# Kernel tuning notes

Hardware: AMD Instinct MI355X
Metric: run time of the kernel (lower is better)

## Reference

```python
import jax, jax.numpy as jnp
import numpy as np

EMB = 1024
NUM_HEADS = 16


def setup_inputs() -> dict:
    key = jax.random.key(0)
    k_x, k_k, k_q, k_v, k_u, k_b = jax.random.split(key, 6)
    b, s, e = 4, 2048, EMB
    lim = 1.0 / np.sqrt(e)
    return {
        "x": jax.random.normal(k_x, (b, s, e), dtype=jnp.float32),
        "Wk": jax.random.uniform(k_k, (e, e), jnp.float32, -lim, lim),
        "Wq": jax.random.uniform(k_q, (e, e), jnp.float32, -lim, lim),
        "Wv": jax.random.uniform(k_v, (e, e), jnp.float32, -lim, lim),
        "Wu": jax.random.uniform(k_u, (e, e), jnp.float32, -lim, lim),
        "bu": jax.random.uniform(k_b, (e,), jnp.float32, -lim, lim),
    }


def reference(x, Wk, Wq, Wv, Wu, bu):
    b, s, e = x.shape
    h = NUM_HEADS
    d = e // h
    # scale q and k each by emb**(-1/4), as in the original (note: emb, not head_size)
    scale = e ** -0.25
    # project and split heads: (b, h, s, d)
    q = (x @ Wq.T).reshape(b, s, h, d).transpose(0, 2, 1, 3) * scale
    k = (x @ Wk.T).reshape(b, s, h, d).transpose(0, 2, 1, 3) * scale
    v = (x @ Wv.T).reshape(b, s, h, d).transpose(0, 2, 1, 3)
    # attention scores (b, h, s, s)
    dot = jnp.einsum("bhqd,bhkd->bhqk", q, k)
    # causal mask: strictly-upper triangle (offset=1) set to -inf
    causal = jnp.triu(jnp.ones((s, s), dtype=bool), k=1)
    dot = jnp.where(causal[None, None, :, :], -jnp.inf, dot)
    attn = jax.nn.softmax(dot, axis=-1)
    out = jnp.einsum("bhqk,bhkd->bhqd", attn, v)
    out = out.transpose(0, 2, 1, 3).reshape(b, s, e)
    return out @ Wu.T + bu
```

## Files before the change

kernel.cpp:

```cpp
#include <hip/hip_runtime.h>
#include <stdint.h>
#include <math.h>


typedef __attribute__((ext_vector_type(8))) short bf16x8;
typedef __attribute__((ext_vector_type(4))) float f32x4;
typedef __attribute__((ext_vector_type(16))) float f32x16;
typedef __attribute__((ext_vector_type(4))) int i32x4;
typedef __attribute__((ext_vector_type(4))) short s16x4;

#define GLOAD_LDS16(gp, lp)                                                     \
  __builtin_amdgcn_global_load_lds(                                             \
      (__attribute__((address_space(1))) void*)(gp),                            \
      (__attribute__((address_space(3))) void*)(lp), 16, 0, 0)

__device__ __forceinline__ short f2bf(float f) {
  union { float f; uint32_t u; } v; v.f = f;
  uint32_t r = v.u + 0x7FFFu + ((v.u >> 16) & 1u);
  return (short)(r >> 16);
}
__device__ __forceinline__ float bf2f(short s) {
  union { uint32_t u; float f; } v; v.u = ((uint32_t)(uint16_t)s) << 16;
  return v.f;
}
__device__ __forceinline__ short f2bfn(float f) {
  union { __bf16 h; short s; } u; u.h = (__bf16)f; return u.s;
}
__device__ __forceinline__ uint32_t pk2n(float a, float b) {
  union { __bf16 h[2]; uint32_t u; } v;
  v.h[0] = (__bf16)a; v.h[1] = (__bf16)b;
  return v.u;
}

__device__ __forceinline__ void swap32(uint32_t a, uint32_t b, int hi,
                                       uint32_t& out0, uint32_t& out1) {
#if __has_builtin(__builtin_amdgcn_permlane32_swap)
  typedef __attribute__((ext_vector_type(2))) int i32x2;
  i32x2 r = __builtin_amdgcn_permlane32_swap((int)a, (int)b, false, false);
  out0 = (uint32_t)r.x; out1 = (uint32_t)r.y;
#else
  uint32_t ta = (uint32_t)__shfl_xor((int)a, 32);
  uint32_t tb = (uint32_t)__shfl_xor((int)b, 32);
  out0 = hi ? tb : a;
  out1 = hi ? b : ta;
#endif
}

__global__ __launch_bounds__(256) void cast_kernel(const float* __restrict__ src,
                                                   short* __restrict__ dst, int n) {
  int i = (blockIdx.x * 256 + threadIdx.x) * 8;
  if (i >= n) return;
  const float4* s = (const float4*)(src + i);
  float4 f0 = s[0], f1 = s[1];
  bf16x8 o;
  o[0] = f2bf(f0.x); o[1] = f2bf(f0.y); o[2] = f2bf(f0.z); o[3] = f2bf(f0.w);
  o[4] = f2bf(f1.x); o[5] = f2bf(f1.y); o[6] = f2bf(f1.z); o[7] = f2bf(f1.w);
  *(bf16x8*)(dst + i) = o;
}

__global__ __launch_bounds__(256) void cast4_kernel(const float* __restrict__ w0,
                                                    const float* __restrict__ w1,
                                                    const float* __restrict__ w2,
                                                    const float* __restrict__ w3,
                                                    short* o0, short* o1, short* o2, short* o3) {
  const float* src = (blockIdx.y == 0) ? w0 : (blockIdx.y == 1) ? w1 : (blockIdx.y == 2) ? w2 : w3;
  short* dst = (blockIdx.y == 0) ? o0 : (blockIdx.y == 1) ? o1 : (blockIdx.y == 2) ? o2 : o3;
  int i = (blockIdx.x * 256 + threadIdx.x) * 8;
  const float4* s = (const float4*)(src + i);
  float4 f0 = s[0], f1 = s[1];
  bf16x8 o;
  o[0] = f2bf(f0.x); o[1] = f2bf(f0.y); o[2] = f2bf(f0.z); o[3] = f2bf(f0.w);
  o[4] = f2bf(f1.x); o[5] = f2bf(f1.y); o[6] = f2bf(f1.z); o[7] = f2bf(f1.w);
  *(bf16x8*)(dst + i) = o;
}

template <bool F32OUT>
__device__ __forceinline__ void gemm_bt_core(const short* __restrict__ A,
                                             const short* __restrict__ Bm,
                                             short* __restrict__ Cb,
                                             float* __restrict__ Cf,
                                             const float* __restrict__ bias) {
  __shared__ short a_lds[128 * 64];
  __shared__ short b_lds[128 * 64];
  const int tid = threadIdx.x;
  const int w = tid >> 6, l = tid & 63;
  const int l15 = l & 15, lhi = l >> 4;
  const int wr = w >> 1, wc = w & 1;
  const int row0 = blockIdx.x * 128;
  const int col0 = blockIdx.y * 128;

  f32x4 acc[4][4];
#pragma unroll
  for (int m = 0; m < 4; ++m)
#pragma unroll
    for (int n = 0; n < 4; ++n)
      acc[m][n] = (f32x4){0.f, 0.f, 0.f, 0.f};

  const int o0 = tid * 16;
  const int sr = o0 >> 7;
  const int sc = o0 & 127;

  for (int kt = 0; kt < 16; ++kt) {
    const char* Ab = (const char*)A + (size_t)(row0 + sr) * 2048 + kt * 128 + sc;
    const char* Bb = (const char*)Bm + (size_t)(col0 + sr) * 2048 + kt * 128 + sc;
#pragma unroll
    for (int i = 0; i < 4; ++i) {
      GLOAD_LDS16(Ab + (size_t)i * 32 * 2048, (char*)a_lds + i * 4096 + o0);
      GLOAD_LDS16(Bb + (size_t)i * 32 * 2048, (char*)b_lds + i * 4096 + o0);
    }
    __syncthreads();
#pragma unroll
    for (int kk = 0; kk < 2; ++kk) {
      bf16x8 af[4], bg[4];
#pragma unroll
      for (int m = 0; m < 4; ++m) {
        int r = wr * 64 + m * 16 + l15;
        af[m] = *(const bf16x8*)((const char*)a_lds + r * 128 + kk * 64 + lhi * 16);
      }
#pragma unroll
      for (int n = 0; n < 4; ++n) {
        int r = wc * 64 + n * 16 + l15;
        bg[n] = *(const bf16x8*)((const char*)b_lds + r * 128 + kk * 64 + lhi * 16);
      }
#pragma unroll
      for (int m = 0; m < 4; ++m)
#pragma unroll
        for (int n = 0; n < 4; ++n)
          acc[m][n] = __builtin_amdgcn_mfma_f32_16x16x32_bf16(af[m], bg[n], acc[m][n], 0, 0, 0);
    }
    __syncthreads();
  }

#pragma unroll
  for (int m = 0; m < 4; ++m) {
#pragma unroll
    for (int n = 0; n < 4; ++n) {
      int colg = col0 + wc * 64 + n * 16 + l15;
#pragma unroll
      for (int r = 0; r < 4; ++r) {
        int rowg = row0 + wr * 64 + m * 16 + lhi * 4 + r;
        float v = acc[m][n][r];
        if constexpr (F32OUT) {
          Cf[(size_t)rowg * 1024 + colg] = v + bias[colg];
        } else {
          Cb[(size_t)rowg * 1024 + colg] = f2bfn(v);
        }
      }
    }
  }
}

__global__ __launch_bounds__(256) void gemm_qkv_kernel(const short* __restrict__ xb,
                                                       const short* __restrict__ wq,
                                                       const short* __restrict__ wk,
                                                       const short* __restrict__ wv,
                                                       short* qo, short* ko, short* vo) {
  const short* Bm = (blockIdx.z == 0) ? wq : (blockIdx.z == 1) ? wk : wv;
  short* C = (blockIdx.z == 0) ? qo : (blockIdx.z == 1) ? ko : vo;
  gemm_bt_core<false>(xb, Bm, C, nullptr, nullptr);
}

__global__ __launch_bounds__(256) void gemm_out_kernel(const short* __restrict__ ob,
                                                       const short* __restrict__ wu,
                                                       const float* __restrict__ bias,
                                                       float* __restrict__ out) {
  gemm_bt_core<true>(ob, wu, nullptr, out, bias);
}

__global__ __launch_bounds__(256) void frag_qk_kernel(const short* __restrict__ qb,
                                                      const short* __restrict__ kb,
                                                      short* __restrict__ qf,
                                                      short* __restrict__ kf) {
  int t = blockIdx.x, bh = blockIdx.y;
  int b = bh >> 4, h = bh & 15;
  __shared__ short q_t[32][72], k_t[32][72];
  int tid = threadIdx.x;
  int row = tid >> 3, seg = tid & 7;
  size_t src = ((size_t)(b * 2048 + t * 32 + row)) * 1024 + h * 64 + seg * 8;
  *(bf16x8*)&q_t[row][seg * 8] = *(const bf16x8*)(qb + src);
  *(bf16x8*)&k_t[row][seg * 8] = *(const bf16x8*)(kb + src);
  __syncthreads();
  int s = tid >> 6, l = tid & 63, l31 = l & 31, hi = l >> 5;
  bf16x8 cq = *(const bf16x8*)&q_t[l31][hi * 8 + s * 16];
  bf16x8 ck = *(const bf16x8*)&k_t[l31][hi * 8 + s * 16];
  size_t dst = ((size_t)bh * 64 + t) * 2048 + s * 512 + l * 8;
  *(bf16x8*)(qf + dst) = cq;
  *(bf16x8*)(kf + dst) = ck;
}

__global__ __launch_bounds__(256) void frag_v_kernel(const short* __restrict__ vb,
                                                     short* __restrict__ vf) {
  int t = blockIdx.x, bh = blockIdx.y;
  int b = bh >> 4, h = bh & 15;
  __shared__ short v_t[32][72];
  int tid = threadIdx.x;
  int row = tid >> 3, seg = tid & 7;
  *(bf16x8*)&v_t[row][seg * 8] =
      *(const bf16x8*)(vb + ((size_t)(b * 2048 + t * 32 + row)) * 1024 + h * 64 + seg * 8);
  __syncthreads();
  int u = tid >> 6, l = tid & 63, l31 = l & 31, hi = l >> 5;
  int dblk = u >> 1, koff = u & 1;
  bf16x8 c;
#pragma unroll
  for (int j = 0; j < 8; ++j) c[j] = v_t[koff * 16 + hi * 8 + j][dblk * 32 + l31];
  *(bf16x8*)(vf + ((size_t)bh * 64 + t) * 2048 + u * 512 + l * 8) = c;
}

__global__ __launch_bounds__(512) void attn_kernel(const short* __restrict__ qf,
                                                   const short* __restrict__ kf,
                                                   const short* __restrict__ vf,
                                                   short* __restrict__ ob) {
  const float QSCALE = 0.03125f * 1.44269504f;
  int bh = blockIdx.x;
  int b = bh >> 4, h = bh & 15;
  int tid = threadIdx.x;
  int wid = tid >> 6, l = tid & 63;
  int l31 = l & 31, hi = l >> 5;
  int pair = blockIdx.y * 4 + (wid >> 1);
  int team = wid & 1;
  int slot = wid >> 1;

  __shared__ float mrg[4][64][34];

  const short* qfb = qf + (size_t)bh * 131072;
  const short* kfb = kf + (size_t)bh * 131072;
  const short* vfb = vf + (size_t)bh * 131072;

  for (int part = 0; part < 2; ++part) {
    int sidx = part ? (63 - pair) : pair;
    int qrow0 = sidx * 32;
    int qg = qrow0 + l31;
    int n = sidx + 1;
    int t0 = team ? (n >> 1) : 0;
    int t1 = team ? n : (n >> 1);

    bf16x8 aq[4];
    {
      const short* qp = qfb + sidx * 2048 + l * 8;
#pragma unroll
      for (int s = 0; s < 4; ++s) {
        bf16x8 t = *(const bf16x8*)(qp + s * 512);
#pragma unroll
        for (int jj = 0; jj < 8; ++jj) t[jj] = f2bfn(bf2f(t[jj]) * QSCALE);
        aq[s] = t;
      }
    }

    f32x16 o_lo = {}, o_hi = {};
    float lsum = 0.f;

    for (int t = t0; t < t1; ++t) {
      const short* kp = kfb + (size_t)t * 2048 + l * 8;
      const short* vp = vfb + (size_t)t * 2048 + l * 8;
      f32x16 st;
#pragma unroll
      for (int r = 0; r < 16; ++r) st[r] = -8.0f;
#pragma unroll
      for (int s = 0; s < 4; ++s) {
        bf16x8 ak = *(const bf16x8*)(kp + s * 512);
        st = __builtin_amdgcn_mfma_f32_32x32x16_bf16(ak, aq[s], st, 0, 0, 0);
      }

      if (t == sidx) {
#pragma unroll
        for (int r = 0; r < 16; ++r) {
          int kk = qrow0 + (r & 3) + 8 * (r >> 2) + 4 * hi;
          if (kk > qg) st[r] = -INFINITY;
        }
      }

#pragma unroll
      for (int r = 0; r < 16; ++r) st[r] = exp2f(st[r]);

      float sm[8];
#pragma unroll
      for (int r = 0; r < 8; ++r) sm[r] = st[r] + st[r + 8];
#pragma unroll
      for (int r = 0; r < 4; ++r) sm[r] += sm[r + 4];
      lsum += (sm[0] + sm[1]) + (sm[2] + sm[3]);

      uint32_t a0, a2, b1, b3, c0, c2, d1, d3;
      swap32(pk2n(st[0], st[1]),   pk2n(st[4], st[5]),   hi, a0, a2);
      swap32(pk2n(st[2], st[3]),   pk2n(st[6], st[7]),   hi, b1, b3);
      swap32(pk2n(st[8], st[9]),   pk2n(st[12], st[13]), hi, c0, c2);
      swap32(pk2n(st[10], st[11]), pk2n(st[14], st[15]), hi, d1, d3);
      i32x4 u0 = {(int)a0, (int)b1, (int)a2, (int)b3};
      i32x4 u1 = {(int)c0, (int)d1, (int)c2, (int)d3};
      bf16x8 pa0 = __builtin_bit_cast(bf16x8, u0);
      bf16x8 pa1 = __builtin_bit_cast(bf16x8, u1);

      bf16x8 av;
      av = *(const bf16x8*)(vp);
      o_lo = __builtin_amdgcn_mfma_f32_32x32x16_bf16(av, pa0, o_lo, 0, 0, 0);
      av = *(const bf16x8*)(vp + 512);
      o_lo = __builtin_amdgcn_mfma_f32_32x32x16_bf16(av, pa1, o_lo, 0, 0, 0);
      av = *(const bf16x8*)(vp + 1024);
      o_hi = __builtin_amdgcn_mfma_f32_32x32x16_bf16(av, pa0, o_hi, 0, 0, 0);
      av = *(const bf16x8*)(vp + 1536);
      o_hi = __builtin_amdgcn_mfma_f32_32x32x16_bf16(av, pa1, o_hi, 0, 0, 0);
    }

    lsum += __shfl_xor(lsum, 32);

    if (team == 1) {
      float* pp = &mrg[slot][l][0];
#pragma unroll
      for (int r = 0; r < 16; ++r) { pp[r] = o_lo[r]; pp[16 + r] = o_hi[r]; }
      pp[32] = lsum;
    }
    __syncthreads();
    if (team == 0) {
      const float* pp = &mrg[slot][l][0];
      float inv = 1.0f / (lsum + pp[32]);
      short* obase = ob + (size_t)(b * 2048 + qg) * 1024 + h * 64;
#pragma unroll
      for (int g = 0; g < 4; ++g) {
        int d0 = 8 * g + 4 * hi;
        s16x4 v0, v1;
#pragma unroll
        for (int jj = 0; jj < 4; ++jj) {
          v0[jj] = f2bfn((o_lo[4 * g + jj] + pp[4 * g + jj]) * inv);
          v1[jj] = f2bfn((o_hi[4 * g + jj] + pp[16 + 4 * g + jj]) * inv);
        }
        *(s16x4*)(obase + d0) = v0;
        *(s16x4*)(obase + 32 + d0) = v1;
      }
    }
    __syncthreads();
  }
}

extern "C" void kernel_launch(void* const* d_in, const int* in_sizes, int n_in,
                              void* d_out, int out_size, void* d_ws, size_t ws_size,
                              hipStream_t stream) {
  const float* x  = (const float*)d_in[0];
  const float* Wk = (const float*)d_in[1];
  const float* Wq = (const float*)d_in[2];
  const float* Wv = (const float*)d_in[3];
  const float* Wu = (const float*)d_in[4];
  const float* bu = (const float*)d_in[5];
  float* out = (float*)d_out;

  char* ws = (char*)d_ws;
  const size_t MB = 1u << 20;
  short* xb  = (short*)(ws + 0 * MB);
  short* qf  = (short*)(ws + 0 * MB);
  short* qb  = (short*)(ws + 16 * MB);
  short* vfb = (short*)(ws + 16 * MB);
  short* kb  = (short*)(ws + 32 * MB);
  short* vb  = (short*)(ws + 48 * MB);
  short* kfb = (short*)(ws + 64 * MB);
  short* ob  = (short*)(ws + 80 * MB);
  short* wqb = (short*)(ws + 96 * MB);
  short* wkb = (short*)(ws + 98 * MB);
  short* wvb = (short*)(ws + 100 * MB);
  short* wub = (short*)(ws + 102 * MB);

  cast_kernel<<<4096, 256, 0, stream>>>(x, xb, 8388608);
  cast4_kernel<<<dim3(512, 4), 256, 0, stream>>>(Wq, Wk, Wv, Wu, wqb, wkb, wvb, wub);

  gemm_qkv_kernel<<<dim3(64, 8, 3), 256, 0, stream>>>(xb, wqb, wkb, wvb, qb, kb, vb);
  frag_qk_kernel<<<dim3(64, 64), 256, 0, stream>>>(qb, kb, qf, kfb);
  frag_v_kernel<<<dim3(64, 64), 256, 0, stream>>>(vb, vfb);
  attn_kernel<<<dim3(64, 8), 512, 0, stream>>>(qf, kfb, vfb, ob);
  gemm_out_kernel<<<dim3(64, 8), 256, 0, stream>>>(ob, wub, bu, out);
}
```

Before: 198.3 us.

## Fuse fragment relayout and Q scaling into QKV GEMM epilogue, prefetch K/V in attention

The QKV GEMM epilogue now writes Q, K and V straight into the MFMA fragment layouts the attention kernel expects, and applies the softmax scale to Q there. This removes the two separate relayout kernels and their extra global round trip, plus the per-element Q rescaling inside attention. The attention loop also software-prefetches the next K tile and loads the V tile before the score MFMAs, so load latency overlaps compute. The cost is scattered 2-byte stores in the GEMM epilogue instead of coalesced row stores, and Q is now rounded to bf16 once after scaling rather than twice.

```diff
diff --git a/kernel.cpp b/kernel.cpp
--- a/kernel.cpp
+++ b/kernel.cpp
@@ -74,12 +74,13 @@
   *(bf16x8*)(dst + i) = o;
 }
 
-template <bool F32OUT>
+template <int MODE>
 __device__ __forceinline__ void gemm_bt_core(const short* __restrict__ A,
                                              const short* __restrict__ Bm,
                                              short* __restrict__ Cb,
                                              float* __restrict__ Cf,
                                              const float* __restrict__ bias) {
+  const float QSCALE = 0.03125f * 1.44269504f;
   __shared__ short a_lds[128 * 64];
   __shared__ short b_lds[128 * 64];
   const int tid = threadIdx.x;
@@ -140,10 +141,24 @@
       for (int r = 0; r < 4; ++r) {
         int rowg = row0 + wr * 64 + m * 16 + lhi * 4 + r;
         float v = acc[m][n][r];
-        if constexpr (F32OUT) {
+        if constexpr (MODE == 3) {
           Cf[(size_t)rowg * 1024 + colg] = v + bias[colg];
         } else {
-          Cb[(size_t)rowg * 1024 + colg] = f2bfn(v);
+          int b = rowg >> 11, srow = rowg & 2047;
+          int t = srow >> 5;
+          int h = colg >> 6, d = colg & 63;
+          size_t base = ((size_t)((b << 4) + h) * 64 + t) << 11;
+          if constexpr (MODE == 2) {
+            int rr = srow & 31;
+            size_t idx = base + (size_t)(((d >> 5) << 1) + (rr >> 4)) * 512 +
+                         (size_t)((((rr >> 3) & 1) << 5) + (d & 31)) * 8 + (rr & 7);
+            Cb[idx] = f2bfn(v);
+          } else {
+            int l31r = srow & 31;
+            size_t idx = base + (size_t)(d >> 4) * 512 +
+                         (size_t)((((d >> 3) & 1) << 5) + l31r) * 8 + (d & 7);
+            Cb[idx] = f2bfn(MODE == 0 ? v * QSCALE : v);
+          }
         }
       }
     }
@@ -154,63 +169,23 @@
                                                        const short* __restrict__ wq,
                                                        const short* __restrict__ wk,
                                                        const short* __restrict__ wv,
-                                                       short* qo, short* ko, short* vo) {
-  const short* Bm = (blockIdx.z == 0) ? wq : (blockIdx.z == 1) ? wk : wv;
-  short* C = (blockIdx.z == 0) ? qo : (blockIdx.z == 1) ? ko : vo;
-  gemm_bt_core<false>(xb, Bm, C, nullptr, nullptr);
+                                                       short* qf, short* kf, short* vf) {
+  if (blockIdx.z == 0)      gemm_bt_core<0>(xb, wq, qf, nullptr, nullptr);
+  else if (blockIdx.z == 1) gemm_bt_core<1>(xb, wk, kf, nullptr, nullptr);
+  else                      gemm_bt_core<2>(xb, wv, vf, nullptr, nullptr);
 }
 
 __global__ __launch_bounds__(256) void gemm_out_kernel(const short* __restrict__ ob,
                                                        const short* __restrict__ wu,
                                                        const float* __restrict__ bias,
                                                        float* __restrict__ out) {
-  gemm_bt_core<true>(ob, wu, nullptr, out, bias);
-}
-
-__global__ __launch_bounds__(256) void frag_qk_kernel(const short* __restrict__ qb,
-                                                      const short* __restrict__ kb,
-                                                      short* __restrict__ qf,
-                                                      short* __restrict__ kf) {
-  int t = blockIdx.x, bh = blockIdx.y;
-  int b = bh >> 4, h = bh & 15;
-  __shared__ short q_t[32][72], k_t[32][72];
-  int tid = threadIdx.x;
-  int row = tid >> 3, seg = tid & 7;
-  size_t src = ((size_t)(b * 2048 + t * 32 + row)) * 1024 + h * 64 + seg * 8;
-  *(bf16x8*)&q_t[row][seg * 8] = *(const bf16x8*)(qb + src);
-  *(bf16x8*)&k_t[row][seg * 8] = *(const bf16x8*)(kb + src);
-  __syncthreads();
-  int s = tid >> 6, l = tid & 63, l31 = l & 31, hi = l >> 5;
-  bf16x8 cq = *(const bf16x8*)&q_t[l31][hi * 8 + s * 16];
-  bf16x8 ck = *(const bf16x8*)&k_t[l31][hi * 8 + s * 16];
-  size_t dst = ((size_t)bh * 64 + t) * 2048 + s * 512 + l * 8;
-  *(bf16x8*)(qf + dst) = cq;
-  *(bf16x8*)(kf + dst) = ck;
-}
-
-__global__ __launch_bounds__(256) void frag_v_kernel(const short* __restrict__ vb,
-                                                     short* __restrict__ vf) {
-  int t = blockIdx.x, bh = blockIdx.y;
-  int b = bh >> 4, h = bh & 15;
-  __shared__ short v_t[32][72];
-  int tid = threadIdx.x;
-  int row = tid >> 3, seg = tid & 7;
-  *(bf16x8*)&v_t[row][seg * 8] =
-      *(const bf16x8*)(vb + ((size_t)(b * 2048 + t * 32 + row)) * 1024 + h * 64 + seg * 8);
-  __syncthreads();
-  int u = tid >> 6, l = tid & 63, l31 = l & 31, hi = l >> 5;
-  int dblk = u >> 1, koff = u & 1;
-  bf16x8 c;
-#pragma unroll
-  for (int j = 0; j < 8; ++j) c[j] = v_t[koff * 16 + hi * 8 + j][dblk * 32 + l31];
-  *(bf16x8*)(vf + ((size_t)bh * 64 + t) * 2048 + u * 512 + l * 8) = c;
+  gemm_bt_core<3>(ob, wu, nullptr, out, bias);
 }
 
 __global__ __launch_bounds__(512) void attn_kernel(const short* __restrict__ qf,
                                                    const short* __restrict__ kf,
                                                    const short* __restrict__ vf,
                                                    short* __restrict__ ob) {
-  const float QSCALE = 0.03125f * 1.44269504f;
   int bh = blockIdx.x;
   int b = bh >> 4, h = bh & 15;
   int tid = threadIdx.x;
@@ -238,66 +213,70 @@
     {
       const short* qp = qfb + sidx * 2048 + l * 8;
 #pragma unroll
-      for (int s = 0; s < 4; ++s) {
-        bf16x8 t = *(const bf16x8*)(qp + s * 512);
-#pragma unroll
-        for (int jj = 0; jj < 8; ++jj) t[jj] = f2bfn(bf2f(t[jj]) * QSCALE);
-        aq[s] = t;
-      }
+      for (int s = 0; s < 4; ++s) aq[s] = *(const bf16x8*)(qp + s * 512);
     }
 
     f32x16 o_lo = {}, o_hi = {};
     float lsum = 0.f;
 
-    for (int t = t0; t < t1; ++t) {
-      const short* kp = kfb + (size_t)t * 2048 + l * 8;
-      const short* vp = vfb + (size_t)t * 2048 + l * 8;
-      f32x16 st;
-#pragma unroll
-      for (int r = 0; r < 16; ++r) st[r] = -8.0f;
-#pragma unroll
-      for (int s = 0; s < 4; ++s) {
-        bf16x8 ak = *(const bf16x8*)(kp + s * 512);
-        st = __builtin_amdgcn_mfma_f32_32x32x16_bf16(ak, aq[s], st, 0, 0, 0);
-      }
-
-      if (t == sidx) {
-#pragma unroll
-        for (int r = 0; r < 16; ++r) {
-          int kk = qrow0 + (r & 3) + 8 * (r >> 2) + 4 * hi;
-          if (kk > qg) st[r] = -INFINITY;
+    if (t0 < t1) {
+      const short* kp = kfb + (size_t)t0 * 2048 + l * 8;
+      const short* vp = vfb + (size_t)t0 * 2048 + l * 8;
+      bf16x8 kc[4];
+#pragma unroll
+      for (int s = 0; s < 4; ++s) kc[s] = *(const bf16x8*)(kp + s * 512);
+
+      for (int t = t0; t < t1; ++t) {
+        bf16x8 vc[4];
+#pragma unroll
+        for (int s = 0; s < 4; ++s) vc[s] = *(const bf16x8*)(vp + s * 512);
+        vp += 2048;
+
+        f32x16 st = {};
+#pragma unroll
+        for (int s = 0; s < 4; ++s)
+          st = __builtin_amdgcn_mfma_f32_32x32x16_bf16(kc[s], aq[s], st, 0, 0, 0);
+
+        kp += 2048;
+        {
+          const short* kpc = (t + 1 < t1) ? kp : (kp - 2048);
+#pragma unroll
+          for (int s = 0; s < 4; ++s) kc[s] = *(const bf16x8*)(kpc + s * 512);
         }
-      }
-
-#pragma unroll
-      for (int r = 0; r < 16; ++r) st[r] = exp2f(st[r]);
-
-      float sm[8];
-#pragma unroll
-      for (int r = 0; r < 8; ++r) sm[r] = st[r] + st[r + 8];
-#pragma unroll
-      for (int r = 0; r < 4; ++r) sm[r] += sm[r + 4];
-      lsum += (sm[0] + sm[1]) + (sm[2] + sm[3]);
-
-      uint32_t a0, a2, b1, b3, c0, c2, d1, d3;
-      swap32(pk2n(st[0], st[1]),   pk2n(st[4], st[5]),   hi, a0, a2);
-      swap32(pk2n(st[2], st[3]),   pk2n(st[6], st[7]),   hi, b1, b3);
-      swap32(pk2n(st[8], st[9]),   pk2n(st[12], st[13]), hi, c0, c2);
-      swap32(pk2n(st[10], st[11]), pk2n(st[14], st[15]), hi, d1, d3);
-      i32x4 u0 = {(int)a0, (int)b1, (int)a2, (int)b3};
-      i32x4 u1 = {(int)c0, (int)d1, (int)c2, (int)d3};
-      bf16x8 pa0 = __builtin_bit_cast(bf16x8, u0);
-      bf16x8 pa1 = __builtin_bit_cast(bf16x8, u1);
-
-      bf16x8 av;
-      av = *(const bf16x8*)(vp);
-      o_lo = __builtin_amdgcn_mfma_f32_32x32x16_bf16(av, pa0, o_lo, 0, 0, 0);
-      av = *(const bf16x8*)(vp + 512);
-      o_lo = __builtin_amdgcn_mfma_f32_32x32x16_bf16(av, pa1, o_lo, 0, 0, 0);
-      av = *(const bf16x8*)(vp + 1024);
-      o_hi = __builtin_amdgcn_mfma_f32_32x32x16_bf16(av, pa0, o_hi, 0, 0, 0);
-      av = *(const bf16x8*)(vp + 1536);
-      o_hi = __builtin_amdgcn_mfma_f32_32x32x16_bf16(av, pa1, o_hi, 0, 0, 0);
+
+        if (t == sidx) {
+#pragma unroll
+          for (int r = 0; r < 16; ++r) {
+            int kk = qrow0 + (r & 3) + 8 * (r >> 2) + 4 * hi;
+            if (kk > qg) st[r] = -INFINITY;
+          }
+        }
+
+#pragma unroll
+        for (int r = 0; r < 16; ++r) st[r] = exp2f(st[r]);
+
+        float sm[8];
+#pragma unroll
+        for (int r = 0; r < 8; ++r) sm[r] = st[r] + st[r + 8];
+#pragma unroll
+        for (int r = 0; r < 4; ++r) sm[r] += sm[r + 4];
+        lsum += (sm[0] + sm[1]) + (sm[2] + sm[3]);
+
+        uint32_t a0, a2, b1, b3, c0, c2, d1, d3;
+        swap32(pk2n(st[0], st[1]),   pk2n(st[4], st[5]),   hi, a0, a2);
+        swap32(pk2n(st[2], st[3]),   pk2n(st[6], st[7]),   hi, b1, b3);
+        swap32(pk2n(st[8], st[9]),   pk2n(st[12], st[13]), hi, c0, c2);
+        swap32(pk2n(st[10], st[11]), pk2n(st[14], st[15]), hi, d1, d3);
+        i32x4 u0 = {(int)a0, (int)b1, (int)a2, (int)b3};
+        i32x4 u1 = {(int)c0, (int)d1, (int)c2, (int)d3};
+        bf16x8 pa0 = __builtin_bit_cast(bf16x8, u0);
+        bf16x8 pa1 = __builtin_bit_cast(bf16x8, u1);
+
+        o_lo = __builtin_amdgcn_mfma_f32_32x32x16_bf16(vc[0], pa0, o_lo, 0, 0, 0);
+        o_lo = __builtin_amdgcn_mfma_f32_32x32x16_bf16(vc[1], pa1, o_lo, 0, 0, 0);
+        o_hi = __builtin_amdgcn_mfma_f32_32x32x16_bf16(vc[2], pa0, o_hi, 0, 0, 0);
+        o_hi = __builtin_amdgcn_mfma_f32_32x32x16_bf16(vc[3], pa1, o_hi, 0, 0, 0);
+      }
     }
 
     lsum += __shfl_xor(lsum, 32);
@@ -344,24 +323,19 @@
   char* ws = (char*)d_ws;
   const size_t MB = 1u << 20;
   short* xb  = (short*)(ws + 0 * MB);
-  short* qf  = (short*)(ws + 0 * MB);
-  short* qb  = (short*)(ws + 16 * MB);
-  short* vfb = (short*)(ws + 16 * MB);
-  short* kb  = (short*)(ws + 32 * MB);
-  short* vb  = (short*)(ws + 48 * MB);
-  short* kfb = (short*)(ws + 64 * MB);
-  short* ob  = (short*)(ws + 80 * MB);
-  short* wqb = (short*)(ws + 96 * MB);
-  short* wkb = (short*)(ws + 98 * MB);
-  short* wvb = (short*)(ws + 100 * MB);
-  short* wub = (short*)(ws + 102 * MB);
+  short* qf  = (short*)(ws + 16 * MB);
+  short* kfb = (short*)(ws + 32 * MB);
+  short* vfb = (short*)(ws + 48 * MB);
+  short* ob  = (short*)(ws + 64 * MB);
+  short* wqb = (short*)(ws + 80 * MB);
+  short* wkb = (short*)(ws + 82 * MB);
+  short* wvb = (short*)(ws + 84 * MB);
+  short* wub = (short*)(ws + 86 * MB);
 
   cast_kernel<<<4096, 256, 0, stream>>>(x, xb, 8388608);
   cast4_kernel<<<dim3(512, 4), 256, 0, stream>>>(Wq, Wk, Wv, Wu, wqb, wkb, wvb, wub);
 
-  gemm_qkv_kernel<<<dim3(64, 8, 3), 256, 0, stream>>>(xb, wqb, wkb, wvb, qb, kb, vb);
-  frag_qk_kernel<<<dim3(64, 64), 256, 0, stream>>>(qb, kb, qf, kfb);
-  frag_v_kernel<<<dim3(64, 64), 256, 0, stream>>>(vb, vfb);
+  gemm_qkv_kernel<<<dim3(64, 8, 3), 256, 0, stream>>>(xb, wqb, wkb, wvb, qf, kfb, vfb);
   attn_kernel<<<dim3(64, 8), 512, 0, stream>>>(qf, kfb, vfb, ob);
   gemm_out_kernel<<<dim3(64, 8), 256, 0, stream>>>(ob, wub, bu, out);
 }
```

Measured after the change: 233.1 us. 17.6% more time.
